# Kernel tuning notes

Measured on AMD Instinct MI355X. Metric: run time of the kernel, lower is better.

The kernel has to match this reference:

```python
import jax, jax.numpy as jnp
import numpy as np

B = 8192  # number of covariance matrices
N = 64    # n_assets


def setup_inputs() -> dict:
    key = jax.random.key(0)
    A = jax.random.normal(key, (B, N, N), dtype=jnp.float32)
    # SPD covariance: A A^T / N + 0.1 I  (real covariances are SPD)
    sigma = jnp.einsum('bij,bkj->bik', A, A) / N + 0.1 * jnp.eye(N, dtype=jnp.float32)
    return {"sigma": sigma}


def reference(sigma) -> jnp.ndarray:
    # Symmetrize, as the original does: 0.5 * (S + S^T)
    sym = 0.5 * (sigma + jnp.swapaxes(sigma, -1, -2))  # [B, N, N]
    n = sym.shape[-1]
    ones = jnp.ones((*sym.shape[:-2], n), dtype=sym.dtype)  # [B, N]
    # Closed-form min-variance (short selling allowed): w = S^-1 1 / (1^T S^-1 1)
    z = jnp.linalg.solve(sym, ones[..., None])[..., 0]      # [B, N]
    w = z / jnp.sum(z, axis=-1, keepdims=True)              # [B, N]
    return w[..., None]  # [B, N, 1], matching expand_dims(axis=-1)
```

## Files before the change

### kernel.cpp

```cpp
#include <hip/hip_runtime.h>


#define NN 64

typedef float v2f __attribute__((ext_vector_type(2)));
typedef float v4f __attribute__((ext_vector_type(4)));

template <int I> struct ic { static constexpr int value = I; };

template <int Start, int End, typename F>
__device__ __forceinline__ void static_for(F&& f) {
    if constexpr (Start < End) {
        f(ic<Start>{});
        static_for<Start + 1, End>(static_cast<F&&>(f));
    }
}

__device__ __forceinline__ float rlane(float v, int lane) {
    return __int_as_float(__builtin_amdgcn_readlane(__float_as_int(v), lane));
}

__device__ __forceinline__ float frcp(float x) {
#if __has_builtin(__builtin_amdgcn_rcpf)
    return __builtin_amdgcn_rcpf(x);
#else
    return 1.0f / x;
#endif
}

__device__ __forceinline__ v2f fma2(v2f a, v2f b, v2f c) {
#if __has_builtin(__builtin_elementwise_fma)
    return __builtin_elementwise_fma(a, b, c);
#else
    v2f r; r.x = fmaf(a.x, b.x, c.x); r.y = fmaf(a.y, b.y, c.y); return r;
#endif
}

__global__ __launch_bounds__(256) void minvar_kernel(const float* __restrict__ sigma,
                                                     float* __restrict__ out,
                                                     int batch) {
    __shared__ v4f buf[4][16];

    const int lane = threadIdx.x & 63;
    const int wid  = threadIdx.x >> 6;
    const int bid  = blockIdx.x * 4 + wid;
    if (bid >= batch) return;

    const float* __restrict__ p = sigma + (size_t)bid * (NN * NN) + (size_t)lane * NN;

    v2f r[NN / 2];
    static_for<0, NN / 4>([&](auto j4c) {
        constexpr int j4 = decltype(j4c)::value;
        v4f v = reinterpret_cast<const v4f*>(p)[j4];
        r[2 * j4 + 0] = v2f{v.x, v.y};
        r[2 * j4 + 1] = v2f{v.z, v.w};
    });

    float b = 1.0f;
    float* __restrict__ fbuf = reinterpret_cast<float*>(&buf[wid][0]);

    static_for<0, NN>([&](auto kc) {
        constexpr int k  = decltype(kc)::value;
        constexpr int c0 = k >> 2;
        constexpr int e0 = k & 3;

        const float colk = (k & 1) ? r[k / 2].y : r[k / 2].x;
        fbuf[lane] = colk;
        __asm__ volatile("s_waitcnt lgkmcnt(0)" ::: "memory");

        const v4f q0 = buf[wid][c0];
        const float pivot = q0[e0];
        const float nf = (lane > k) ? (-colk * frcp(pivot)) : 0.0f;
        b = fmaf(nf, rlane(b, k), b);
        const v2f nf2 = v2f{nf, nf};

        r[2 * c0 + 0] = fma2(nf2, v2f{q0.x, q0.y}, r[2 * c0 + 0]);
        r[2 * c0 + 1] = fma2(nf2, v2f{q0.z, q0.w}, r[2 * c0 + 1]);

        static_for<0, 4>([&](auto gc) {
            constexpr int g = decltype(gc)::value;
            if constexpr (4 * g + 3 > c0) {
                v4f q[4];
                static_for<0, 4>([&](auto tc) {
                    constexpr int t = decltype(tc)::value;
                    if constexpr (4 * g + t > c0) q[t] = buf[wid][4 * g + t];
                });
                static_for<0, 4>([&](auto tc) {
                    constexpr int t = decltype(tc)::value;
                    constexpr int c = 4 * g + t;
                    if constexpr (c > c0) {
                        r[2 * c + 0] = fma2(nf2, v2f{q[t].x, q[t].y}, r[2 * c + 0]);
                        r[2 * c + 1] = fma2(nf2, v2f{q[t].z, q[t].w}, r[2 * c + 1]);
                    }
                });
            }
        });
    });

    static_for<0, NN>([&](auto kk) {
        constexpr int k  = NN - 1 - decltype(kk)::value;
        constexpr int pk = k / 2;
        const float ekk  = (k & 1) ? r[pk].y : r[pk].x;
        const float ukk  = rlane(ekk, k);
        const float yk   = rlane(b, k);
        const float zk   = yk * frcp(ukk);
        const float upd  = (lane < k) ? (-ekk) : 0.0f;
        b = (lane == k) ? zk : fmaf(upd, zk, b);
    });

    float tot = b;
    #pragma unroll
    for (int off = 32; off >= 1; off >>= 1)
        tot += __shfl_xor(tot, off, 64);

    out[(size_t)bid * NN + lane] = b * frcp(tot);
}

extern "C" void kernel_launch(void* const* d_in, const int* in_sizes, int n_in,
                              void* d_out, int out_size, void* d_ws, size_t ws_size,
                              hipStream_t stream) {
    const float* sigma = (const float*)d_in[0];
    float* out = (float*)d_out;
    const int batch  = in_sizes[0] / (NN * NN);
    const int blocks = (batch + 3) / 4;
    minvar_kernel<<<blocks, 256, 0, stream>>>(sigma, out, batch);
}
```

Baseline: 203.1 us.

## Block Gaussian elimination by four pivots with readlane panel and interleaved LDS broadcast

The elimination now handles pivots in panels of four. Inside a panel, pivot rows are read with readlane instead of LDS, and each lane writes its four panel column entries once, interleaved in LDS so that two v4f loads per column pair give all four pivot-row values. The trailing update then applies four rank-1 updates per LDS read. This cuts the per-pivot LDS store/wait round trips from 64 to 15 and raises arithmetic per LDS load. The cost is a serial chain of readlanes inside each panel and a double-buffered LDS region per wave, which needs no explicit wait.

```diff
diff --git a/kernel.cpp b/kernel.cpp
--- a/kernel.cpp
+++ b/kernel.cpp
@@ -39,7 +39,7 @@
 __global__ __launch_bounds__(256) void minvar_kernel(const float* __restrict__ sigma,
                                                      float* __restrict__ out,
                                                      int batch) {
-    __shared__ v4f buf[4][16];
+    __shared__ float pb[4][2][2 * NN * 4 / 2];
 
     const int lane = threadIdx.x & 63;
     const int wid  = threadIdx.x >> 6;
@@ -57,54 +57,76 @@
     });
 
     float b = 1.0f;
-    float* __restrict__ fbuf = reinterpret_cast<float*>(&buf[wid][0]);
+    const int wbase = (lane >> 1) * 8 + (lane & 1);
 
-    static_for<0, NN>([&](auto kc) {
-        constexpr int k  = decltype(kc)::value;
-        constexpr int c0 = k >> 2;
-        constexpr int e0 = k & 3;
+    static_for<0, 16>([&](auto pc) {
+        constexpr int P  = decltype(pc)::value;
+        constexpr int k0 = 4 * P;
+        constexpr int m0 = 2 * P;
+        float* __restrict__ wb = &pb[wid][P & 1][0];
 
-        const float colk = (k & 1) ? r[k / 2].y : r[k / 2].x;
-        fbuf[lane] = colk;
-        __asm__ volatile("s_waitcnt lgkmcnt(0)" ::: "memory");
+        const float el0  = r[m0].x;
+        const float piv0 = rlane(el0, k0);
+        const float nf0  = (lane > k0) ? (-el0 * frcp(piv0)) : 0.0f;
+        b = fmaf(nf0, rlane(b, k0), b);
+        const float u01 = rlane(r[m0].y,     k0);
+        const float u02 = rlane(r[m0 + 1].x, k0);
+        const float u03 = rlane(r[m0 + 1].y, k0);
+        r[m0].y     = fmaf(nf0, u01, r[m0].y);
+        r[m0 + 1].x = fmaf(nf0, u02, r[m0 + 1].x);
+        r[m0 + 1].y = fmaf(nf0, u03, r[m0 + 1].y);
 
-        const v4f q0 = buf[wid][c0];
-        const float pivot = q0[e0];
-        const float nf = (lane > k) ? (-colk * frcp(pivot)) : 0.0f;
-        b = fmaf(nf, rlane(b, k), b);
-        const v2f nf2 = v2f{nf, nf};
+        const float el1  = r[m0].y;
+        const float piv1 = rlane(el1, k0 + 1);
+        const float nf1  = (lane > k0 + 1) ? (-el1 * frcp(piv1)) : 0.0f;
+        b = fmaf(nf1, rlane(b, k0 + 1), b);
+        const float u12 = rlane(r[m0 + 1].x, k0 + 1);
+        const float u13 = rlane(r[m0 + 1].y, k0 + 1);
+        r[m0 + 1].x = fmaf(nf1, u12, r[m0 + 1].x);
+        r[m0 + 1].y = fmaf(nf1, u13, r[m0 + 1].y);
 
-        r[2 * c0 + 0] = fma2(nf2, v2f{q0.x, q0.y}, r[2 * c0 + 0]);
-        r[2 * c0 + 1] = fma2(nf2, v2f{q0.z, q0.w}, r[2 * c0 + 1]);
+        const float el2  = r[m0 + 1].x;
+        const float piv2 = rlane(el2, k0 + 2);
+        const float nf2  = (lane > k0 + 2) ? (-el2 * frcp(piv2)) : 0.0f;
+        b = fmaf(nf2, rlane(b, k0 + 2), b);
+        const float u23 = rlane(r[m0 + 1].y, k0 + 2);
+        r[m0 + 1].y = fmaf(nf2, u23, r[m0 + 1].y);
 
-        static_for<0, 4>([&](auto gc) {
-            constexpr int g = decltype(gc)::value;
-            if constexpr (4 * g + 3 > c0) {
-                v4f q[4];
-                static_for<0, 4>([&](auto tc) {
-                    constexpr int t = decltype(tc)::value;
-                    if constexpr (4 * g + t > c0) q[t] = buf[wid][4 * g + t];
-                });
-                static_for<0, 4>([&](auto tc) {
-                    constexpr int t = decltype(tc)::value;
-                    constexpr int c = 4 * g + t;
-                    if constexpr (c > c0) {
-                        r[2 * c + 0] = fma2(nf2, v2f{q[t].x, q[t].y}, r[2 * c + 0]);
-                        r[2 * c + 1] = fma2(nf2, v2f{q[t].z, q[t].w}, r[2 * c + 1]);
-                    }
-                });
-            }
-        });
+        const float el3  = r[m0 + 1].y;
+        const float piv3 = rlane(el3, k0 + 3);
+        const float nf3  = (lane > k0 + 3) ? (-el3 * frcp(piv3)) : 0.0f;
+        b = fmaf(nf3, rlane(b, k0 + 3), b);
+
+        if constexpr (P < 15) {
+            wb[wbase + 0] = el0;
+            wb[wbase + 2] = el1;
+            wb[wbase + 4] = el2;
+            wb[wbase + 6] = el3;
+
+            const v2f n0 = v2f{nf0, nf0}, n1 = v2f{nf1, nf1};
+            const v2f n2 = v2f{nf2, nf2}, n3 = v2f{nf3, nf3};
+            static_for<m0 + 2, NN / 2>([&](auto mc) {
+                constexpr int m = decltype(mc)::value;
+                const v4f lo = *reinterpret_cast<const v4f*>(wb + 8 * m);
+                const v4f hi = *reinterpret_cast<const v4f*>(wb + 8 * m + 4);
+                v2f acc = r[m];
+                acc = fma2(n0, v2f{lo.x, lo.y}, acc);
+                acc = fma2(n1, v2f{lo.z, lo.w}, acc);
+                acc = fma2(n2, v2f{hi.x, hi.y}, acc);
+                acc = fma2(n3, v2f{hi.z, hi.w}, acc);
+                r[m] = acc;
+            });
+        }
     });
 
     static_for<0, NN>([&](auto kk) {
         constexpr int k  = NN - 1 - decltype(kk)::value;
         constexpr int pk = k / 2;
-        const float ekk  = (k & 1) ? r[pk].y : r[pk].x;
-        const float ukk  = rlane(ekk, k);
-        const float yk   = rlane(b, k);
-        const float zk   = yk * frcp(ukk);
-        const float upd  = (lane < k) ? (-ekk) : 0.0f;
+        const float ekk = (k & 1) ? r[pk].y : r[pk].x;
+        const float ukk = rlane(ekk, k);
+        const float yk  = rlane(b, k);
+        const float zk  = yk * frcp(ukk);
+        const float upd = (lane < k) ? (-ekk) : 0.0f;
         b = (lane == k) ? zk : fmaf(upd, zk, b);
     });
 
```

Result: no change. 201.4 us (-0.8%).
